# Performance work log

Hardware: AMD Instinct MI355X
Metric: run time of the kernel (lower is better)

## Reference

```python
import jax, jax.numpy as jnp
import numpy as np

EPS = 1e-5

def _bilinear_sample(xb, ys, xs):
    # xb: [C,H,W]; ys, xs: [H,W] float sample coordinates (zero outside bounds)
    C, H, W = xb.shape
    y0 = jnp.floor(ys); x0 = jnp.floor(xs)
    y1 = y0 + 1.0;      x1 = x0 + 1.0
    wy1 = ys - y0; wy0 = 1.0 - wy1
    wx1 = xs - x0; wx0 = 1.0 - wx1
    def g(yi, xi):
        valid = (yi >= 0) & (yi < H) & (xi >= 0) & (xi < W)
        yc = jnp.clip(yi, 0, H - 1).astype(jnp.int32)
        xc = jnp.clip(xi, 0, W - 1).astype(jnp.int32)
        return xb[:, yc, xc] * valid[None].astype(xb.dtype)  # [C,H,W]
    return (g(y0, x0) * (wy0 * wx0)[None] + g(y0, x1) * (wy0 * wx1)[None]
          + g(y1, x0) * (wy1 * wx0)[None] + g(y1, x1) * (wy1 * wx1)[None])

def _deform_conv2d(x, offset, mask, w, b):
    # x:[B,C,H,W] offset:[B,18,H,W] mask:[B,9,H,W] w:[Co,C,3,3] b:[Co]
    B, C, H, W = x.shape
    Co = w.shape[0]
    ii = jnp.arange(H, dtype=x.dtype)[:, None]
    jj = jnp.arange(W, dtype=x.dtype)[None, :]
    cols = []
    for k in range(9):  # fixed 3x3 kernel positions, row-major (dy=offset[2k], dx=offset[2k+1])
        ky, kx = k // 3 - 1, k % 3 - 1
        ys = ii + ky + offset[:, 2 * k]      # [B,H,W]
        xs = jj + kx + offset[:, 2 * k + 1]
        v = jax.vmap(_bilinear_sample)(x, ys, xs)  # [B,C,H,W]
        cols.append(v * mask[:, k][:, None])
    cols = jnp.stack(cols, axis=1)               # [B,9,C,H,W]
    out = jnp.einsum('bkchw,ock->bohw', cols, w.reshape(Co, C, 9))
    return out + b[None, :, None, None]

def setup_inputs() -> dict:
    key = jax.random.key(0)
    k1, k2, k3, k4 = jax.random.split(key, 4)
    B, Cin, Cout, H, W = 8, 64, 64, 128, 128
    x = jax.random.normal(k1, (B, Cin, H, W), dtype=jnp.float32)
    # offset/mask conv: small weights so learned offsets stay O(1) pixels;
    # bias[18:]=2.0 as in the module's init (masks start near sigmoid(2))
    w_off = jax.random.normal(k2, (27, Cin, 3, 3), dtype=jnp.float32) * 0.01
    b_off = jnp.concatenate([jnp.zeros((18,), jnp.float32), jnp.full((9,), 2.0, jnp.float32)])
    w_dcn = jax.random.normal(k3, (Cout, Cin, 3, 3), dtype=jnp.float32) / np.sqrt(Cin * 9)
    b_dcn = jax.random.normal(k4, (Cout,), dtype=jnp.float32) * 0.01
    return {"x": x, "w_off": w_off, "b_off": b_off, "w_dcn": w_dcn, "b_dcn": b_dcn}

def reference(x, w_off, b_off, w_dcn, b_dcn):
    dn = ('NCHW', 'OIHW', 'NCHW')
    om = jax.lax.conv_general_dilated(x, w_off, (1, 1), 'SAME', dimension_numbers=dn)
    om = om + b_off[None, :, None, None]
    offset = om[:, :18]
    mask = jax.nn.sigmoid(om[:, 18:])
    y = _deform_conv2d(x, offset, mask, w_dcn, b_dcn)
    # InstanceNorm2d (affine=False, biased variance) + ReLU
    mu = jnp.mean(y, axis=(2, 3), keepdims=True)
    var = jnp.var(y, axis=(2, 3), keepdims=True)
    y = (y - mu) * jax.lax.rsqrt(var + EPS)
    return jax.nn.relu(y)
```

## Files before the change

kernel.cpp:

```cpp
#include <hip/hip_runtime.h>
#include <hip/hip_fp16.h>

#define BB   8
#define CIN  64
#define COUT 64
#define HH   128
#define WW   128
#define HWSZ (HH * WW)

typedef _Float16 f16x8 __attribute__((ext_vector_type(8)));
typedef _Float16 h2v   __attribute__((ext_vector_type(2)));
typedef float    f32x4 __attribute__((ext_vector_type(4)));

__device__ __forceinline__ unsigned short f2h_u(float f) {
    __half h = __float2half(f);
    return __half_as_ushort(h);
}
__device__ __forceinline__ unsigned duph(float f) {
    unsigned u = (unsigned)f2h_u(f);
    return u | (u << 16);
}

__device__ __forceinline__ unsigned comb2h(unsigned a, unsigned b, unsigned c, unsigned d,
                                           h2v W0, h2v W1, h2v W2, h2v W3) {
    h2v A = *(h2v*)&a, B = *(h2v*)&b, C = *(h2v*)&c, D = *(h2v*)&d;
    h2v r = A * W0;
    r += B * W1;
    r += C * W2;
    r += D * W3;
    return *(unsigned*)&r;
}


__global__ __launch_bounds__(256) void k_tr(const float* __restrict__ x,
                                            const float* __restrict__ wd,
                                            const float* __restrict__ wof,
                                            unsigned short* __restrict__ xT,
                                            unsigned short* __restrict__ wdT,
                                            unsigned short* __restrict__ wofT,
                                            float4* __restrict__ sums4)
{
    const int t = threadIdx.x;
    const int id = blockIdx.x;
    if (id >= 512) {
        if (id == 512) sums4[t] = make_float4(0.f, 0.f, 0.f, 0.f);
        int base = (id - 512) * 256 + t;
#pragma unroll
        for (int j = 0; j < 4; ++j) {
            int idx = base + j * 16384;
            if (idx < 36864) {
                int k = idx >> 12, rem = idx & 4095, co = rem >> 6, c = rem & 63;
                wdT[idx] = f2h_u(wd[(co * 64 + c) * 9 + k]);
            } else if (idx < 55296) {
                int jj = idx - 36864;
                int k = jj >> 11, rem = jj & 2047, o = rem >> 6, c = rem & 63;
                wofT[jj] = (o < 27) ? f2h_u(wof[(o * 64 + c) * 9 + k]) : 0;
            }
        }
        return;
    }
    __shared__ unsigned short tile[256 * 66];
    const int b = id & 7;
    const int p0 = (id >> 3) * 256;
#pragma unroll
    for (int i = 0; i < 16; ++i) {
        int c = i * 4 + (t >> 6);
        int pl = (t & 63) * 4;
        float4 v = *(const float4*)(x + (((size_t)b * 64 + c) << 14) + p0 + pl);
        tile[(pl + 0) * 66 + c] = f2h_u(v.x);
        tile[(pl + 1) * 66 + c] = f2h_u(v.y);
        tile[(pl + 2) * 66 + c] = f2h_u(v.z);
        tile[(pl + 3) * 66 + c] = f2h_u(v.w);
    }
    __syncthreads();
#pragma unroll
    for (int i = 0; i < 8; ++i) {
        int idd = i * 256 + t;
        int pt = idd >> 3, ck = idd & 7;
        const unsigned* srcp = (const unsigned*)&tile[pt * 66 + ck * 8];
        uint4 r;
        r.x = srcp[0]; r.y = srcp[1]; r.z = srcp[2]; r.w = srcp[3];
        *(uint4*)(xT + ((size_t)b << 20) + ((size_t)(ck >> 2) << 19)
                     + (size_t)(p0 + pt) * 32 + (ck & 3) * 8) = r;
    }
}

__global__ __launch_bounds__(256, 2) void k_off(
    const unsigned short* __restrict__ xT, const unsigned short* __restrict__ wofT,
    const float* __restrict__ bof, float* __restrict__ om)
{
    __shared__ unsigned short tile[8 * 521 * 8];
    const int t = threadIdx.x;
    const int lane = t & 63, wv = t >> 6;
    const int q = lane >> 4, l15 = lane & 15;
    const int b = blockIdx.x & 7;
    const int xblk = blockIdx.x >> 3;
    const int h0 = xblk * 2;
    const int r0 = h0 - 1;
    const unsigned short* xb = xT + ((size_t)b << 20);

#pragma unroll
    for (int i = 0; i < 17; ++i) {
        int id = i * 256 + t;
        if (id < 4160) {
            int m = id & 7, lin = id >> 3;
            int row = lin / 130, col = lin % 130;
            int gy = r0 + row, gx = col - 1;
            uint4 v = {0u, 0u, 0u, 0u};
            if (((unsigned)gy < (unsigned)HH) && ((unsigned)gx < (unsigned)WW))
                v = *(const uint4*)(xb + ((size_t)(m >> 2) << 19)
                                       + (size_t)(gy * WW + gx) * 32 + (m & 3) * 8);
            *(uint4*)&tile[(m * 521 + lin) * 8] = v;
        }
    }
    __syncthreads();

    const int hrow = h0 + (wv >> 1);
    const int c0 = (wv & 1) * 64;

    f32x4 acc[2][4];
#pragma unroll
    for (int mt = 0; mt < 2; ++mt)
#pragma unroll
        for (int nt = 0; nt < 4; ++nt) acc[mt][nt] = (f32x4){0.f, 0.f, 0.f, 0.f};

#pragma unroll
    for (int k = 0; k < 9; ++k) {
        const int ky = k / 3 - 1, kx = k % 3 - 1;
        const int trow = (hrow - h0) + ky + 1;
        const unsigned short* wk = wofT + k * 2048;
#pragma unroll
        for (int ks = 0; ks < 2; ++ks) {
            f16x8 af[2], bfr[4];
#pragma unroll
            for (int mt = 0; mt < 2; ++mt)
                af[mt] = *(const f16x8*)(wk + (mt * 16 + l15) * 64 + ks * 32 + q * 8);
#pragma unroll
            for (int nt = 0; nt < 4; ++nt) {
                int tc = c0 + nt * 16 + l15 + kx + 1;
                bfr[nt] = *(const f16x8*)&tile[((ks * 4 + q) * 521 + trow * 130 + tc) * 8];
            }
#pragma unroll
            for (int mt = 0; mt < 2; ++mt)
#pragma unroll
                for (int nt = 0; nt < 4; ++nt)
                    acc[mt][nt] = __builtin_amdgcn_mfma_f32_16x16x32_f16(
                        af[mt], bfr[nt], acc[mt][nt], 0, 0, 0);
        }
    }

    const int p0 = xblk * 256 + wv * 64;
    float* omb = om + (size_t)b * 27 * HWSZ;
#pragma unroll
    for (int mt = 0; mt < 2; ++mt)
#pragma unroll
        for (int r = 0; r < 4; ++r) {
            int o = mt * 16 + q * 4 + r;
            if (o < 27) {
                float bias = bof[o];
#pragma unroll
                for (int nt = 0; nt < 4; ++nt) {
                    int pp = p0 + nt * 16 + l15;
                    float v = acc[mt][nt][r] + bias;
                    if (o >= 18) v = 1.f / (1.f + __expf(-v));
                    omb[(size_t)o * HWSZ + pp] = v;
                }
            }
        }
}

__global__ __launch_bounds__(256, 2) void k_dcn(
    const unsigned short* __restrict__ xT, const float* __restrict__ om,
    const unsigned short* __restrict__ wdT, const float* __restrict__ bd,
    float* __restrict__ out, float2* __restrict__ sums)
{
    __shared__ unsigned short tile_sh[6 * 128 * 32];
    __shared__ unsigned short col_sh[4][64 * 40];
    __shared__ unsigned       adr_sh[4][4][64];
    __shared__ uint4          w_sh[4][64];
    __shared__ float          redS[4][64];
    __shared__ float          redQ[4][64];

    const int t = threadIdx.x;
    const int lane = t & 63, wv = t >> 6;
    const int q = lane >> 4, l15 = lane & 15;
    const int b = blockIdx.x & 7;
    const int pblk = (blockIdx.x >> 3) * 256;
    const int p = pblk + t;
    const int h = p >> 7, w = p & 127;
    const int h0 = pblk >> 7;
    const unsigned short* xbS = xT + ((size_t)b << 20);
    const float* omp = om + (size_t)b * 27 * HWSZ + p;
    const int gpt = lane >> 2;
    const int gch = (lane & 3) * 8;

    f32x4 acc[4][4];
#pragma unroll
    for (int mt = 0; mt < 4; ++mt)
#pragma unroll
        for (int nt = 0; nt < 4; ++nt) acc[mt][nt] = (f32x4){0.f, 0.f, 0.f, 0.f};

#define LOADG(P, g) { \
    int pt_ = (g) * 16 + gpt; \
    P[0] = *(const uint4*)&tile_sh[(adr_sh[wv][0][pt_] & 0x7fffu) + gch]; \
    P[1] = *(const uint4*)&tile_sh[(adr_sh[wv][1][pt_] & 0x7fffu) + gch]; \
    P[2] = *(const uint4*)&tile_sh[(adr_sh[wv][2][pt_] & 0x7fffu) + gch]; \
    P[3] = *(const uint4*)&tile_sh[(adr_sh[wv][3][pt_] & 0x7fffu) + gch]; }

#define COMBG(P, g) { \
    int pt_ = (g) * 16 + gpt; \
    uint4 pw_ = w_sh[wv][pt_]; \
    h2v W0_ = *(h2v*)&pw_.x, W1_ = *(h2v*)&pw_.y; \
    h2v W2_ = *(h2v*)&pw_.z, W3_ = *(h2v*)&pw_.w; \
    uint4 R_; \
    R_.x = comb2h(P[0].x, P[1].x, P[2].x, P[3].x, W0_, W1_, W2_, W3_); \
    R_.y = comb2h(P[0].y, P[1].y, P[2].y, P[3].y, W0_, W1_, W2_, W3_); \
    R_.z = comb2h(P[0].z, P[1].z, P[2].z, P[3].z, W0_, W1_, W2_, W3_); \
    R_.w = comb2h(P[0].w, P[1].w, P[2].w, P[3].w, W0_, W1_, W2_, W3_); \
    *(uint4*)&col_sh[wv][pt_ * 40 + gch] = R_; }

    for (int hf = 0; hf < 2; ++hf) {
        __syncthreads();
        const unsigned short* xbh = xbS + (hf << 19);
#pragma unroll
        for (int i = 0; i < 12; ++i) {
            int idx = i * 256 + t;
            int s = idx >> 9, u = idx & 511;
            int y = h0 - 2 + s;
            y = min(max(y, 0), HH - 1);
            uint4 v = *(const uint4*)(xbh + (size_t)y * (WW * 32) + u * 8);
            *(uint4*)&tile_sh[idx * 8] = v;
        }
        __syncthreads();

        float offy = omp[0];
        float offx = omp[HWSZ];
        float mk   = omp[18 * HWSZ];

        for (int k = 0; k < 9; ++k) {
            float ys = (float)(h + (k / 3) - 1) + offy;
            float xs = (float)(w + (k % 3) - 1) + offx;
            float fy0 = floorf(ys), fx0 = floorf(xs);
            float wy1 = ys - fy0, wx1 = xs - fx0;
            float wy0 = 1.f - wy1, wx0 = 1.f - wx1;
            int y0 = (int)fy0, x0 = (int)fx0;
            int y1 = y0 + 1, x1 = x0 + 1;
            bool vy0 = (y0 >= 0) && (y0 < HH), vy1 = (y1 >= 0) && (y1 < HH);
            bool vx0 = (x0 >= 0) && (x0 < WW), vx1 = (x1 >= 0) && (x1 < WW);
            int y0c = min(max(y0, 0), HH - 1), y1c = min(max(y1, 0), HH - 1);
            int x0c = min(max(x0, 0), WW - 1), x1c = min(max(x1, 0), WW - 1);
            bool ft = (y0c < h0 - 2) || (y1c > h0 + 3);
            unsigned a0, a1, a2, a3;
            if (!ft) {
                int r0s = (y0c - h0 + 2) * (WW * 32);
                int r1s = (y1c - h0 + 2) * (WW * 32);
                a0 = (unsigned)(r0s + x0c * 32);
                a1 = (unsigned)(r0s + x1c * 32);
                a2 = (unsigned)(r1s + x0c * 32);
                a3 = (unsigned)(r1s + x1c * 32);
            } else {
                unsigned fb = 0x80000000u;
                a0 = fb | (unsigned)((y0c * WW + x0c) * 32);
                a1 = fb | (unsigned)((y0c * WW + x1c) * 32);
                a2 = fb | (unsigned)((y1c * WW + x0c) * 32);
                a3 = fb | (unsigned)((y1c * WW + x1c) * 32);
            }
            adr_sh[wv][0][lane] = a0;
            adr_sh[wv][1][lane] = a1;
            adr_sh[wv][2][lane] = a2;
            adr_sh[wv][3][lane] = a3;
            uint4 pw = make_uint4(
                duph((vy0 && vx0) ? mk * wy0 * wx0 : 0.f),
                duph((vy0 && vx1) ? mk * wy0 * wx1 : 0.f),
                duph((vy1 && vx0) ? mk * wy1 * wx0 : 0.f),
                duph((vy1 && vx1) ? mk * wy1 * wx1 : 0.f));
            w_sh[wv][lane] = pw;
            int kn = (k < 8) ? k + 1 : 8;
            offy = omp[(2 * kn) * HWSZ];
            offx = omp[(2 * kn + 1) * HWSZ];
            mk   = omp[(18 + kn) * HWSZ];
            __builtin_amdgcn_wave_barrier();

            uint4 pb[3][4];
            LOADG(pb[0], 0);
            LOADG(pb[1], 1);
#pragma unroll
            for (int g = 0; g < 4; ++g) {
                if (g + 2 < 4) LOADG(pb[(g + 2) % 3], g + 2);
                COMBG(pb[g % 3], g);
            }

            if (ft) {
                const unsigned short* c0 = xbh + (y0c * WW + x0c) * 32;
                const unsigned short* c1 = xbh + (y0c * WW + x1c) * 32;
                const unsigned short* c2 = xbh + (y1c * WW + x0c) * 32;
                const unsigned short* c3 = xbh + (y1c * WW + x1c) * 32;
                h2v W0 = *(h2v*)&pw.x, W1 = *(h2v*)&pw.y;
                h2v W2 = *(h2v*)&pw.z, W3 = *(h2v*)&pw.w;
#pragma unroll
                for (int j = 0; j < 4; ++j) {
                    uint4 A  = *(const uint4*)(c0 + j * 8);
                    uint4 Bv = *(const uint4*)(c1 + j * 8);
                    uint4 Cv = *(const uint4*)(c2 + j * 8);
                    uint4 Dv = *(const uint4*)(c3 + j * 8);
                    uint4 R;
                    R.x = comb2h(A.x, Bv.x, Cv.x, Dv.x, W0, W1, W2, W3);
                    R.y = comb2h(A.y, Bv.y, Cv.y, Dv.y, W0, W1, W2, W3);
                    R.z = comb2h(A.z, Bv.z, Cv.z, Dv.z, W0, W1, W2, W3);
                    R.w = comb2h(A.w, Bv.w, Cv.w, Dv.w, W0, W1, W2, W3);
                    *(uint4*)&col_sh[wv][lane * 40 + j * 8] = R;
                }
            }
            __builtin_amdgcn_wave_barrier();

            const unsigned short* wk = wdT + k * 4096;
            f16x8 af_[4];
#pragma unroll
            for (int mt = 0; mt < 4; ++mt)
                af_[mt] = *(const f16x8*)(wk + (mt * 16 + l15) * 64 + (hf << 5) + q * 8);
            f16x8 bfr[4];
#pragma unroll
            for (int nt = 0; nt < 4; ++nt)
                bfr[nt] = *(const f16x8*)&col_sh[wv][(nt * 16 + l15) * 40 + q * 8];
#pragma unroll
            for (int mt = 0; mt < 4; ++mt)
#pragma unroll
                for (int nt = 0; nt < 4; ++nt)
                    acc[mt][nt] = __builtin_amdgcn_mfma_f32_16x16x32_f16(
                        af_[mt], bfr[nt], acc[mt][nt], 0, 0, 0);
        }
    }
#undef LOADG
#undef COMBG

    const int p0 = pblk + wv * 64;
    float* outb = out + (size_t)b * COUT * HWSZ;
#pragma unroll
    for (int mt = 0; mt < 4; ++mt)
#pragma unroll
        for (int r = 0; r < 4; ++r) {
            int co = mt * 16 + q * 4 + r;
            float bias = bd[co];
            float s = 0.f, qq = 0.f;
#pragma unroll
            for (int nt = 0; nt < 4; ++nt) {
                float v = acc[mt][nt][r] + bias;
                outb[(size_t)co * HWSZ + p0 + nt * 16 + l15] = v;
                s += v; qq += v * v;
            }
#pragma unroll
            for (int m = 1; m < 16; m <<= 1) {
                s += __shfl_xor(s, m);
                qq += __shfl_xor(qq, m);
            }
            if (l15 == 0) { redS[wv][co] = s; redQ[wv][co] = qq; }
        }
    __syncthreads();
    if (t < 64) {
        float S = redS[0][t] + redS[1][t] + redS[2][t] + redS[3][t];
        float Q = redQ[0][t] + redQ[1][t] + redQ[2][t] + redQ[3][t];
        atomicAdd(&sums[b * 64 + t].x, S);
        atomicAdd(&sums[b * 64 + t].y, Q);
    }
}

__global__ __launch_bounds__(256) void k_norm(float* __restrict__ out,
                                              const float2* __restrict__ sums)
{
    const int id = blockIdx.x;
    const int b = id & 7;
    const int rest = id >> 3;
    const int co = rest >> 4;
    const int off = rest & 15;
    const int bco = b * 64 + co;
    const int i = (bco << 12) + off * 256 + threadIdx.x;
    float2 sq = sums[bco];
    float mu  = sq.x * (1.f / (float)HWSZ);
    float var = sq.y * (1.f / (float)HWSZ) - mu * mu;
    float rstd = rsqrtf(var + 1e-5f);
    float4* o4 = (float4*)out;
    float4 v = o4[i];
    v.x = fmaxf((v.x - mu) * rstd, 0.f);
    v.y = fmaxf((v.y - mu) * rstd, 0.f);
    v.z = fmaxf((v.z - mu) * rstd, 0.f);
    v.w = fmaxf((v.w - mu) * rstd, 0.f);
    o4[i] = v;
}

extern "C" void kernel_launch(void* const* d_in, const int* in_sizes, int n_in,
                              void* d_out, int out_size, void* d_ws, size_t ws_size,
                              hipStream_t stream) {
    const float* x   = (const float*)d_in[0];
    const float* wof = (const float*)d_in[1];
    const float* bof = (const float*)d_in[2];
    const float* wd  = (const float*)d_in[3];
    const float* bd  = (const float*)d_in[4];
    float* out = (float*)d_out;

    char* ws = (char*)d_ws;
    unsigned short* xT   = (unsigned short*)ws;
    float*          om   = (float*)(ws + 16777216);
    unsigned short* wdT  = (unsigned short*)(ws + 30932992);
    unsigned short* wofT = (unsigned short*)(ws + 31006720);
    float2*         sums = (float2*)(ws + 31043584);

    k_tr    <<<576, 256, 0, stream>>>(x, wd, wof, xT, wdT, wofT, (float4*)sums);
    k_off   <<<512, 256, 0, stream>>>(xT, wofT, bof, om);
    k_dcn   <<<512, 256, 0, stream>>>(xT, om, wdT, bd, out, sums);
    k_norm  <<<8192, 256, 0, stream>>>(out, (const float2*)sums);
}
```

Measured before the change: 158.4 us.

## Build MFMA B-operand fragments directly in registers, removing col_sh staging

Each lane now gathers bilinear corner samples into the exact layout of the MFMA B fragment (point l15, channel group q) and feeds the combined fp16 result straight to the MFMA, so the column tile is no longer staged in shared memory. This removes the col_sh write/read round trip, one wave barrier and the separate fallback pass over out-of-tile points, which now take a per-group branch to global memory instead. It also frees LDS, but adds per-lane branch divergence when some points in a 16-point group fall outside the tile.

```diff
diff --git a/kernel.cpp b/kernel.cpp
--- a/kernel.cpp
+++ b/kernel.cpp
@@ -175,7 +175,6 @@
     float* __restrict__ out, float2* __restrict__ sums)
 {
     __shared__ unsigned short tile_sh[6 * 128 * 32];
-    __shared__ unsigned short col_sh[4][64 * 40];
     __shared__ unsigned       adr_sh[4][4][64];
     __shared__ uint4          w_sh[4][64];
     __shared__ float          redS[4][64];
@@ -191,25 +190,29 @@
     const int h0 = pblk >> 7;
     const unsigned short* xbS = xT + ((size_t)b << 20);
     const float* omp = om + (size_t)b * 27 * HWSZ + p;
-    const int gpt = lane >> 2;
-    const int gch = (lane & 3) * 8;
+    const int gch = q * 8;
 
     f32x4 acc[4][4];
 #pragma unroll
     for (int mt = 0; mt < 4; ++mt)
 #pragma unroll
-        for (int nt = 0; nt < 4; ++nt) acc[mt][nt] = (f32x4){0.f, 0.f, 0.f, 0.f};
-
-#define LOADG(P, g) { \
-    int pt_ = (g) * 16 + gpt; \
-    P[0] = *(const uint4*)&tile_sh[(adr_sh[wv][0][pt_] & 0x7fffu) + gch]; \
-    P[1] = *(const uint4*)&tile_sh[(adr_sh[wv][1][pt_] & 0x7fffu) + gch]; \
-    P[2] = *(const uint4*)&tile_sh[(adr_sh[wv][2][pt_] & 0x7fffu) + gch]; \
-    P[3] = *(const uint4*)&tile_sh[(adr_sh[wv][3][pt_] & 0x7fffu) + gch]; }
-
-#define COMBG(P, g) { \
-    int pt_ = (g) * 16 + gpt; \
-    uint4 pw_ = w_sh[wv][pt_]; \
+        for (int g = 0; g < 4; ++g) acc[mt][g] = (f32x4){0.f, 0.f, 0.f, 0.f};
+
+#define LOADG2(P, g) { \
+    if (__builtin_expect((int)(ga[g][0] >> 31), 0)) { \
+        P[0] = *(const uint4*)(xbh + (ga[g][0] & 0x7fffffffu) + gch); \
+        P[1] = *(const uint4*)(xbh + (ga[g][1] & 0x7fffffffu) + gch); \
+        P[2] = *(const uint4*)(xbh + (ga[g][2] & 0x7fffffffu) + gch); \
+        P[3] = *(const uint4*)(xbh + (ga[g][3] & 0x7fffffffu) + gch); \
+    } else { \
+        P[0] = *(const uint4*)&tile_sh[(ga[g][0] & 0x7fffu) + gch]; \
+        P[1] = *(const uint4*)&tile_sh[(ga[g][1] & 0x7fffu) + gch]; \
+        P[2] = *(const uint4*)&tile_sh[(ga[g][2] & 0x7fffu) + gch]; \
+        P[3] = *(const uint4*)&tile_sh[(ga[g][3] & 0x7fffu) + gch]; \
+    } }
+
+#define COMB2(DST, P, g) { \
+    uint4 pw_ = gw[g]; \
     h2v W0_ = *(h2v*)&pw_.x, W1_ = *(h2v*)&pw_.y; \
     h2v W2_ = *(h2v*)&pw_.z, W3_ = *(h2v*)&pw_.w; \
     uint4 R_; \
@@ -217,7 +220,7 @@
     R_.y = comb2h(P[0].y, P[1].y, P[2].y, P[3].y, W0_, W1_, W2_, W3_); \
     R_.z = comb2h(P[0].z, P[1].z, P[2].z, P[3].z, W0_, W1_, W2_, W3_); \
     R_.w = comb2h(P[0].w, P[1].w, P[2].w, P[3].w, W0_, W1_, W2_, W3_); \
-    *(uint4*)&col_sh[wv][pt_ * 40 + gch] = R_; }
+    DST = *(f16x8*)&R_; }
 
     for (int hf = 0; hf < 2; ++hf) {
         __syncthreads();
@@ -269,69 +272,55 @@
             adr_sh[wv][1][lane] = a1;
             adr_sh[wv][2][lane] = a2;
             adr_sh[wv][3][lane] = a3;
-            uint4 pw = make_uint4(
+            w_sh[wv][lane] = make_uint4(
                 duph((vy0 && vx0) ? mk * wy0 * wx0 : 0.f),
                 duph((vy0 && vx1) ? mk * wy0 * wx1 : 0.f),
                 duph((vy1 && vx0) ? mk * wy1 * wx0 : 0.f),
                 duph((vy1 && vx1) ? mk * wy1 * wx1 : 0.f));
-            w_sh[wv][lane] = pw;
             int kn = (k < 8) ? k + 1 : 8;
             offy = omp[(2 * kn) * HWSZ];
             offx = omp[(2 * kn + 1) * HWSZ];
             mk   = omp[(18 + kn) * HWSZ];
             __builtin_amdgcn_wave_barrier();
 
-            uint4 pb[3][4];
-            LOADG(pb[0], 0);
-            LOADG(pb[1], 1);
+            unsigned ga[4][4];
+            uint4 gw[4];
 #pragma unroll
             for (int g = 0; g < 4; ++g) {
-                if (g + 2 < 4) LOADG(pb[(g + 2) % 3], g + 2);
-                COMBG(pb[g % 3], g);
-            }
-
-            if (ft) {
-                const unsigned short* c0 = xbh + (y0c * WW + x0c) * 32;
-                const unsigned short* c1 = xbh + (y0c * WW + x1c) * 32;
-                const unsigned short* c2 = xbh + (y1c * WW + x0c) * 32;
-                const unsigned short* c3 = xbh + (y1c * WW + x1c) * 32;
-                h2v W0 = *(h2v*)&pw.x, W1 = *(h2v*)&pw.y;
-                h2v W2 = *(h2v*)&pw.z, W3 = *(h2v*)&pw.w;
-#pragma unroll
-                for (int j = 0; j < 4; ++j) {
-                    uint4 A  = *(const uint4*)(c0 + j * 8);
-                    uint4 Bv = *(const uint4*)(c1 + j * 8);
-                    uint4 Cv = *(const uint4*)(c2 + j * 8);
-                    uint4 Dv = *(const uint4*)(c3 + j * 8);
-                    uint4 R;
-                    R.x = comb2h(A.x, Bv.x, Cv.x, Dv.x, W0, W1, W2, W3);
-                    R.y = comb2h(A.y, Bv.y, Cv.y, Dv.y, W0, W1, W2, W3);
-                    R.z = comb2h(A.z, Bv.z, Cv.z, Dv.z, W0, W1, W2, W3);
-                    R.w = comb2h(A.w, Bv.w, Cv.w, Dv.w, W0, W1, W2, W3);
-                    *(uint4*)&col_sh[wv][lane * 40 + j * 8] = R;
-                }
-            }
-            __builtin_amdgcn_wave_barrier();
+                int pt_ = g * 16 + l15;
+                ga[g][0] = adr_sh[wv][0][pt_];
+                ga[g][1] = adr_sh[wv][1][pt_];
+                ga[g][2] = adr_sh[wv][2][pt_];
+                ga[g][3] = adr_sh[wv][3][pt_];
+                gw[g] = w_sh[wv][pt_];
+            }
 
             const unsigned short* wk = wdT + k * 4096;
             f16x8 af_[4];
 #pragma unroll
             for (int mt = 0; mt < 4; ++mt)
                 af_[mt] = *(const f16x8*)(wk + (mt * 16 + l15) * 64 + (hf << 5) + q * 8);
+
             f16x8 bfr[4];
-#pragma unroll
-            for (int nt = 0; nt < 4; ++nt)
-                bfr[nt] = *(const f16x8*)&col_sh[wv][(nt * 16 + l15) * 40 + q * 8];
+            uint4 pb[3][4];
+            LOADG2(pb[0], 0);
+            LOADG2(pb[1], 1);
+#pragma unroll
+            for (int g = 0; g < 4; ++g) {
+                if (g + 2 < 4) LOADG2(pb[(g + 2) % 3], g + 2);
+                COMB2(bfr[g], pb[g % 3], g);
+            }
+
 #pragma unroll
             for (int mt = 0; mt < 4; ++mt)
 #pragma unroll
-                for (int nt = 0; nt < 4; ++nt)
-                    acc[mt][nt] = __builtin_amdgcn_mfma_f32_16x16x32_f16(
-                        af_[mt], bfr[nt], acc[mt][nt], 0, 0, 0);
-        }
-    }
-#undef LOADG
-#undef COMBG
+                for (int g = 0; g < 4; ++g)
+                    acc[mt][g] = __builtin_amdgcn_mfma_f32_16x16x32_f16(
+                        af_[mt], bfr[g], acc[mt][g], 0, 0, 0);
+        }
+    }
+#undef LOADG2
+#undef COMB2
 
     const int p0 = pblk + wv * 64;
     float* outb = out + (size_t)b * COUT * HWSZ;
@@ -343,9 +332,9 @@
             float bias = bd[co];
             float s = 0.f, qq = 0.f;
 #pragma unroll
-            for (int nt = 0; nt < 4; ++nt) {
-                float v = acc[mt][nt][r] + bias;
-                outb[(size_t)co * HWSZ + p0 + nt * 16 + l15] = v;
+            for (int g = 0; g < 4; ++g) {
+                float v = acc[mt][g][r] + bias;
+                outb[(size_t)co * HWSZ + p0 + g * 16 + l15] = v;
                 s += v; qq += v * v;
             }
 #pragma unroll
```

Result: faster. 151.7 us (-4.2%).
